# Optimization experiments

Measured on AMD Instinct MI355X. Metric: run time of the kernel, lower is better.

Reference implementation:

```python
import jax, jax.numpy as jnp
import numpy as np

D = 16  # feature (height) dim fixed by nn.Linear(16,16)

def setup_inputs() -> dict:
    key = jax.random.key(0)
    ks = jax.random.split(key, 7)
    B, C = 32, 1024
    inp = jax.random.normal(ks[0], (B, C, D), dtype=jnp.float32)
    s = 1.0 / np.sqrt(D)
    Wq = jax.random.uniform(ks[1], (D, D), jnp.float32, -s, s)
    bq = jax.random.uniform(ks[2], (D,), jnp.float32, -s, s)
    Wk = jax.random.uniform(ks[3], (D, D), jnp.float32, -s, s)
    bk = jax.random.uniform(ks[4], (D,), jnp.float32, -s, s)
    Wv = jax.random.uniform(ks[5], (D, D), jnp.float32, -s, s)
    bv = jax.random.uniform(ks[6], (D,), jnp.float32, -s, s)
    return {"input": inp, "Wq": Wq, "bq": bq, "Wk": Wk, "bk": bk, "Wv": Wv, "bv": bv}

def reference(input, Wq, bq, Wk, bk, Wv, bv):
    # torch Linear: y = x @ W.T + b
    Q = jnp.einsum('bcd,ed->bce', input, Wq) + bq  # [B,C,16]
    K = jnp.einsum('bcd,ed->bce', input, Wk) + bk
    V = jnp.einsum('bcd,ed->bce', input, Wv) + bv
    W = jnp.einsum('bqd,bkd->bqk', Q, K)           # [B,C,C], unscaled
    W = jax.nn.softmax(W, axis=2)
    att = jnp.einsum('bqk,bkd->bqd', W, V)         # [B,C,16]
    return att * input                              # elementwise gate
```

## Files before the change

### kernel.cpp

```cpp
#include <hip/hip_runtime.h>
#include <math.h>

#define DD 16
#define CC 1024
#define BB 32
#define QT 32

__global__ __launch_bounds__(256) void qkv_kernel(
    const float* __restrict__ x,
    const float* __restrict__ Wq, const float* __restrict__ bq,
    const float* __restrict__ Wk, const float* __restrict__ bk,
    const float* __restrict__ Wv, const float* __restrict__ bv,
    float* __restrict__ Q, float* __restrict__ K, float* __restrict__ V)
{
    __shared__ float xs[256 * DD];
    const int tid = threadIdx.x;
    const int m = blockIdx.y;
    const float* W    = (m == 0) ? Wq : (m == 1) ? Wk : Wv;
    const float* bias = (m == 0) ? bq : (m == 1) ? bk : bv;
    float*       O    = (m == 0) ? Q  : (m == 1) ? K  : V;

    const long base4 = (long)blockIdx.x * 256 * 4;
    const float4* x4 = (const float4*)x;
    float4* xs4 = (float4*)xs;
#pragma unroll
    for (int i = 0; i < 4; ++i)
        xs4[i * 256 + tid] = x4[base4 + i * 256 + tid];
    __syncthreads();

    float xr[16];
#pragma unroll
    for (int i = 0; i < 4; ++i) {
        float4 t = xs4[tid * 4 + i];
        xr[i*4+0] = t.x; xr[i*4+1] = t.y; xr[i*4+2] = t.z; xr[i*4+3] = t.w;
    }

    const long row = (long)blockIdx.x * 256 + tid;
    float4* O4 = (float4*)O;
#pragma unroll
    for (int g = 0; g < 4; ++g) {
        float o[4];
#pragma unroll
        for (int j = 0; j < 4; ++j) {
            const int e = g * 4 + j;
            float a = bias[e];
            const float* w = W + e * 16;
#pragma unroll
            for (int d = 0; d < 16; ++d) a = fmaf(xr[d], w[d], a);
            o[j] = a;
        }
        float4 ov; ov.x = o[0]; ov.y = o[1]; ov.z = o[2]; ov.w = o[3];
        O4[row * 4 + g] = ov;
    }
}

__global__ __launch_bounds__(256, 4) void attn_kernel(
    const float* __restrict__ Q, const float* __restrict__ K,
    const float* __restrict__ V, const float* __restrict__ x,
    float* __restrict__ out)
{
    __shared__ float smem[8192 + 256];
    float4* Ks4 = (float4*)smem;
    float4* Vs4 = (float4*)(smem + 4096);

    const int tid = threadIdx.x;
    const int q   = tid & 31;
    const int ks  = tid >> 5;
    const int b   = blockIdx.y;
    const int qbase = blockIdx.x * QT;
    const long qrow = (long)b * CC + qbase + q;

    const float4* Q4 = (const float4*)Q;
    float qr[16];
#pragma unroll
    for (int i = 0; i < 4; ++i) {
        float4 t = Q4[qrow * 4 + i];
        qr[i*4+0] = t.x; qr[i*4+1] = t.y; qr[i*4+2] = t.z; qr[i*4+3] = t.w;
    }

    float l = 0.f;
    float acc[16];
#pragma unroll
    for (int d = 0; d < 16; ++d) acc[d] = 0.f;

    const float4* K4 = (const float4*)K;
    const float4* V4 = (const float4*)V;

    for (int t = 0; t < 4; ++t) {
        const long tb4 = ((long)b * CC + t * 256) * 4;
        __syncthreads();
#pragma unroll
        for (int i = 0; i < 4; ++i) {
            Ks4[i * 256 + tid] = K4[tb4 + i * 256 + tid];
            Vs4[i * 256 + tid] = V4[tb4 + i * 256 + tid];
        }
        __syncthreads();

        const int k0 = ks * 32;
#pragma unroll 4
        for (int kk = 0; kk < 32; ++kk) {
            const int k = k0 + kk;
            float4 ka = Ks4[k * 4 + 0];
            float4 kb = Ks4[k * 4 + 1];
            float4 kc = Ks4[k * 4 + 2];
            float4 kd = Ks4[k * 4 + 3];
            float s = qr[0] * ka.x;
            s = fmaf(qr[1],  ka.y, s); s = fmaf(qr[2],  ka.z, s); s = fmaf(qr[3],  ka.w, s);
            s = fmaf(qr[4],  kb.x, s); s = fmaf(qr[5],  kb.y, s); s = fmaf(qr[6],  kb.z, s); s = fmaf(qr[7],  kb.w, s);
            s = fmaf(qr[8],  kc.x, s); s = fmaf(qr[9],  kc.y, s); s = fmaf(qr[10], kc.z, s); s = fmaf(qr[11], kc.w, s);
            s = fmaf(qr[12], kd.x, s); s = fmaf(qr[13], kd.y, s); s = fmaf(qr[14], kd.z, s); s = fmaf(qr[15], kd.w, s);

            const float p = __expf(s);
            l += p;

            float4 va = Vs4[k * 4 + 0];
            float4 vb = Vs4[k * 4 + 1];
            float4 vc = Vs4[k * 4 + 2];
            float4 vd = Vs4[k * 4 + 3];
            acc[0]  = fmaf(p, va.x, acc[0]);  acc[1]  = fmaf(p, va.y, acc[1]);
            acc[2]  = fmaf(p, va.z, acc[2]);  acc[3]  = fmaf(p, va.w, acc[3]);
            acc[4]  = fmaf(p, vb.x, acc[4]);  acc[5]  = fmaf(p, vb.y, acc[5]);
            acc[6]  = fmaf(p, vb.z, acc[6]);  acc[7]  = fmaf(p, vb.w, acc[7]);
            acc[8]  = fmaf(p, vc.x, acc[8]);  acc[9]  = fmaf(p, vc.y, acc[9]);
            acc[10] = fmaf(p, vc.z, acc[10]); acc[11] = fmaf(p, vc.w, acc[11]);
            acc[12] = fmaf(p, vd.x, acc[12]); acc[13] = fmaf(p, vd.y, acc[13]);
            acc[14] = fmaf(p, vd.z, acc[14]); acc[15] = fmaf(p, vd.w, acc[15]);
        }
    }

    __syncthreads();
    float* As = smem;
    float* Ls = smem + 8192;
    float4* As4 = (float4*)As;
#pragma unroll
    for (int i = 0; i < 4; ++i) {
        float4 t4;
        t4.x = acc[i*4+0]; t4.y = acc[i*4+1]; t4.z = acc[i*4+2]; t4.w = acc[i*4+3];
        As4[tid * 4 + i] = t4;
    }
    Ls[tid] = l;
    __syncthreads();

    if (tid < 128) {
        const int qq = tid & 31;
        const int dg = tid >> 5;
        float L = 0.f;
        float4 o; o.x = 0.f; o.y = 0.f; o.z = 0.f; o.w = 0.f;
#pragma unroll
        for (int s = 0; s < 8; ++s) {
            L += Ls[s * 32 + qq];
            float4 a = As4[(s * 32 + qq) * 4 + dg];
            o.x += a.x; o.y += a.y; o.z += a.z; o.w += a.w;
        }
        const float invL = 1.f / L;
        const long orow = (long)b * CC + qbase + qq;
        const float4 xg = ((const float4*)x)[orow * 4 + dg];
        float4 r;
        r.x = o.x * invL * xg.x;
        r.y = o.y * invL * xg.y;
        r.z = o.z * invL * xg.z;
        r.w = o.w * invL * xg.w;
        ((float4*)out)[orow * 4 + dg] = r;
    }
}

extern "C" void kernel_launch(void* const* d_in, const int* in_sizes, int n_in,
                              void* d_out, int out_size, void* d_ws, size_t ws_size,
                              hipStream_t stream) {
    const float* x  = (const float*)d_in[0];
    const float* Wq = (const float*)d_in[1];
    const float* bq = (const float*)d_in[2];
    const float* Wk = (const float*)d_in[3];
    const float* bk = (const float*)d_in[4];
    const float* Wv = (const float*)d_in[5];
    const float* bv = (const float*)d_in[6];
    float* out = (float*)d_out;

    const long n = (long)BB * CC * DD;
    float* Q = (float*)d_ws;
    float* K = Q + n;
    float* V = K + n;

    qkv_kernel<<<dim3((BB * CC) / 256, 3), dim3(256), 0, stream>>>(
        x, Wq, bq, Wk, bk, Wv, bv, Q, K, V);

    attn_kernel<<<dim3(CC / QT, BB), dim3(256), 0, stream>>>(Q, K, V, x, out);
}
```

Baseline: 116.3 us.

## Register-block four queries per thread and widen attention blocks to 512 threads

Each thread now keeps four query rows in registers, so every K and V row read from shared memory feeds four dot products and four accumulator updates instead of one. Blocks grow to 512 threads and 128 queries, with the 16 key-split warps walking keys in an interleaved order. This cuts LDS traffic per FLOP and reloads each K/V tile for fewer, larger blocks. In exchange it raises register pressure (64 accumulators plus 64 query values per thread), halves the occupancy hint, and turns the final reduction into four serialized shared-memory passes.

```diff
diff --git a/kernel.cpp b/kernel.cpp
--- a/kernel.cpp
+++ b/kernel.cpp
@@ -4,7 +4,8 @@
 #define DD 16
 #define CC 1024
 #define BB 32
-#define QT 32
+#define QT 128
+#define KT 256
 
 __global__ __launch_bounds__(256) void qkv_kernel(
     const float* __restrict__ x,
@@ -54,113 +55,135 @@
     }
 }
 
-__global__ __launch_bounds__(256, 4) void attn_kernel(
+__global__ __launch_bounds__(512, 2) void attn_kernel(
     const float* __restrict__ Q, const float* __restrict__ K,
     const float* __restrict__ V, const float* __restrict__ x,
     float* __restrict__ out)
 {
-    __shared__ float smem[8192 + 256];
+    __shared__ float smem[8192 + 512];
     float4* Ks4 = (float4*)smem;
     float4* Vs4 = (float4*)(smem + 4096);
 
     const int tid = threadIdx.x;
-    const int q   = tid & 31;
+    const int q32 = tid & 31;
     const int ks  = tid >> 5;
     const int b   = blockIdx.y;
     const int qbase = blockIdx.x * QT;
-    const long qrow = (long)b * CC + qbase + q;
 
     const float4* Q4 = (const float4*)Q;
-    float qr[16];
-#pragma unroll
-    for (int i = 0; i < 4; ++i) {
-        float4 t = Q4[qrow * 4 + i];
-        qr[i*4+0] = t.x; qr[i*4+1] = t.y; qr[i*4+2] = t.z; qr[i*4+3] = t.w;
-    }
-
-    float l = 0.f;
-    float acc[16];
-#pragma unroll
-    for (int d = 0; d < 16; ++d) acc[d] = 0.f;
+    float qr[4][16];
+#pragma unroll
+    for (int qb = 0; qb < 4; ++qb) {
+        const long row = (long)b * CC + qbase + qb * 32 + q32;
+#pragma unroll
+        for (int i = 0; i < 4; ++i) {
+            float4 t = Q4[row * 4 + i];
+            qr[qb][i*4+0] = t.x; qr[qb][i*4+1] = t.y;
+            qr[qb][i*4+2] = t.z; qr[qb][i*4+3] = t.w;
+        }
+    }
+
+    float lsum[4];
+    float acc[4][16];
+#pragma unroll
+    for (int qb = 0; qb < 4; ++qb) {
+        lsum[qb] = 0.f;
+#pragma unroll
+        for (int d = 0; d < 16; ++d) acc[qb][d] = 0.f;
+    }
 
     const float4* K4 = (const float4*)K;
     const float4* V4 = (const float4*)V;
 
     for (int t = 0; t < 4; ++t) {
-        const long tb4 = ((long)b * CC + t * 256) * 4;
-        __syncthreads();
-#pragma unroll
-        for (int i = 0; i < 4; ++i) {
-            Ks4[i * 256 + tid] = K4[tb4 + i * 256 + tid];
-            Vs4[i * 256 + tid] = V4[tb4 + i * 256 + tid];
-        }
-        __syncthreads();
-
-        const int k0 = ks * 32;
+        const long tb4 = ((long)b * CC + t * KT) * 4;
+        __syncthreads();
+        Ks4[tid]       = K4[tb4 + tid];
+        Ks4[tid + 512] = K4[tb4 + tid + 512];
+        Vs4[tid]       = V4[tb4 + tid];
+        Vs4[tid + 512] = V4[tb4 + tid + 512];
+        __syncthreads();
+
 #pragma unroll 4
-        for (int kk = 0; kk < 32; ++kk) {
-            const int k = k0 + kk;
-            float4 ka = Ks4[k * 4 + 0];
-            float4 kb = Ks4[k * 4 + 1];
-            float4 kc = Ks4[k * 4 + 2];
-            float4 kd = Ks4[k * 4 + 3];
-            float s = qr[0] * ka.x;
-            s = fmaf(qr[1],  ka.y, s); s = fmaf(qr[2],  ka.z, s); s = fmaf(qr[3],  ka.w, s);
-            s = fmaf(qr[4],  kb.x, s); s = fmaf(qr[5],  kb.y, s); s = fmaf(qr[6],  kb.z, s); s = fmaf(qr[7],  kb.w, s);
-            s = fmaf(qr[8],  kc.x, s); s = fmaf(qr[9],  kc.y, s); s = fmaf(qr[10], kc.z, s); s = fmaf(qr[11], kc.w, s);
-            s = fmaf(qr[12], kd.x, s); s = fmaf(qr[13], kd.y, s); s = fmaf(qr[14], kd.z, s); s = fmaf(qr[15], kd.w, s);
-
-            const float p = __expf(s);
-            l += p;
-
-            float4 va = Vs4[k * 4 + 0];
-            float4 vb = Vs4[k * 4 + 1];
-            float4 vc = Vs4[k * 4 + 2];
-            float4 vd = Vs4[k * 4 + 3];
-            acc[0]  = fmaf(p, va.x, acc[0]);  acc[1]  = fmaf(p, va.y, acc[1]);
-            acc[2]  = fmaf(p, va.z, acc[2]);  acc[3]  = fmaf(p, va.w, acc[3]);
-            acc[4]  = fmaf(p, vb.x, acc[4]);  acc[5]  = fmaf(p, vb.y, acc[5]);
-            acc[6]  = fmaf(p, vb.z, acc[6]);  acc[7]  = fmaf(p, vb.w, acc[7]);
-            acc[8]  = fmaf(p, vc.x, acc[8]);  acc[9]  = fmaf(p, vc.y, acc[9]);
-            acc[10] = fmaf(p, vc.z, acc[10]); acc[11] = fmaf(p, vc.w, acc[11]);
-            acc[12] = fmaf(p, vd.x, acc[12]); acc[13] = fmaf(p, vd.y, acc[13]);
-            acc[14] = fmaf(p, vd.z, acc[14]); acc[15] = fmaf(p, vd.w, acc[15]);
-        }
-    }
-
-    __syncthreads();
+        for (int kk = 0; kk < 16; ++kk) {
+            const int kl = (kk << 4) + ks;
+            const float4 ka = Ks4[kl * 4 + 0];
+            const float4 kb = Ks4[kl * 4 + 1];
+            const float4 kc = Ks4[kl * 4 + 2];
+            const float4 kd = Ks4[kl * 4 + 3];
+            float kr[16];
+            kr[0]=ka.x; kr[1]=ka.y; kr[2]=ka.z; kr[3]=ka.w;
+            kr[4]=kb.x; kr[5]=kb.y; kr[6]=kb.z; kr[7]=kb.w;
+            kr[8]=kc.x; kr[9]=kc.y; kr[10]=kc.z; kr[11]=kc.w;
+            kr[12]=kd.x; kr[13]=kd.y; kr[14]=kd.z; kr[15]=kd.w;
+
+            float p[4];
+#pragma unroll
+            for (int qb = 0; qb < 4; ++qb) {
+                float s = qr[qb][0] * kr[0];
+#pragma unroll
+                for (int d = 1; d < 16; ++d) s = fmaf(qr[qb][d], kr[d], s);
+                p[qb] = __expf(s);
+                lsum[qb] += p[qb];
+            }
+
+            const float4 va = Vs4[kl * 4 + 0];
+            const float4 vb = Vs4[kl * 4 + 1];
+            const float4 vc = Vs4[kl * 4 + 2];
+            const float4 vd = Vs4[kl * 4 + 3];
+            float vr[16];
+            vr[0]=va.x; vr[1]=va.y; vr[2]=va.z; vr[3]=va.w;
+            vr[4]=vb.x; vr[5]=vb.y; vr[6]=vb.z; vr[7]=vb.w;
+            vr[8]=vc.x; vr[9]=vc.y; vr[10]=vc.z; vr[11]=vc.w;
+            vr[12]=vd.x; vr[13]=vd.y; vr[14]=vd.z; vr[15]=vd.w;
+#pragma unroll
+            for (int qb = 0; qb < 4; ++qb)
+#pragma unroll
+                for (int d = 0; d < 16; ++d)
+                    acc[qb][d] = fmaf(p[qb], vr[d], acc[qb][d]);
+        }
+    }
+
     float* As = smem;
     float* Ls = smem + 8192;
     float4* As4 = (float4*)As;
-#pragma unroll
-    for (int i = 0; i < 4; ++i) {
-        float4 t4;
-        t4.x = acc[i*4+0]; t4.y = acc[i*4+1]; t4.z = acc[i*4+2]; t4.w = acc[i*4+3];
-        As4[tid * 4 + i] = t4;
-    }
-    Ls[tid] = l;
-    __syncthreads();
-
-    if (tid < 128) {
-        const int qq = tid & 31;
-        const int dg = tid >> 5;
-        float L = 0.f;
-        float4 o; o.x = 0.f; o.y = 0.f; o.z = 0.f; o.w = 0.f;
-#pragma unroll
-        for (int s = 0; s < 8; ++s) {
-            L += Ls[s * 32 + qq];
-            float4 a = As4[(s * 32 + qq) * 4 + dg];
-            o.x += a.x; o.y += a.y; o.z += a.z; o.w += a.w;
-        }
-        const float invL = 1.f / L;
-        const long orow = (long)b * CC + qbase + qq;
-        const float4 xg = ((const float4*)x)[orow * 4 + dg];
-        float4 r;
-        r.x = o.x * invL * xg.x;
-        r.y = o.y * invL * xg.y;
-        r.z = o.z * invL * xg.z;
-        r.w = o.w * invL * xg.w;
-        ((float4*)out)[orow * 4 + dg] = r;
+    const float4* x4 = (const float4*)x;
+    float4* out4 = (float4*)out;
+
+#pragma unroll
+    for (int qb = 0; qb < 4; ++qb) {
+        __syncthreads();
+#pragma unroll
+        for (int i = 0; i < 4; ++i) {
+            float4 t4;
+            t4.x = acc[qb][i*4+0]; t4.y = acc[qb][i*4+1];
+            t4.z = acc[qb][i*4+2]; t4.w = acc[qb][i*4+3];
+            As4[tid * 4 + i] = t4;
+        }
+        Ls[tid] = lsum[qb];
+        __syncthreads();
+
+        if (tid < 128) {
+            const int qq = tid >> 2;
+            const int dg = tid & 3;
+            float L = 0.f;
+            float4 o; o.x = 0.f; o.y = 0.f; o.z = 0.f; o.w = 0.f;
+#pragma unroll
+            for (int s = 0; s < 16; ++s) {
+                L += Ls[s * 32 + qq];
+                float4 a = As4[(s * 32 + qq) * 4 + dg];
+                o.x += a.x; o.y += a.y; o.z += a.z; o.w += a.w;
+            }
+            const float invL = 1.f / L;
+            const long orow = (long)b * CC + qbase + qb * 32 + qq;
+            const float4 xg = x4[orow * 4 + dg];
+            float4 r;
+            r.x = o.x * invL * xg.x;
+            r.y = o.y * invL * xg.y;
+            r.z = o.z * invL * xg.z;
+            r.w = o.w * invL * xg.w;
+            out4[orow * 4 + dg] = r;
+        }
     }
 }
 
@@ -184,5 +207,5 @@
     qkv_kernel<<<dim3((BB * CC) / 256, 3), dim3(256), 0, stream>>>(
         x, Wq, bq, Wk, bk, Wv, bv, Q, K, V);
 
-    attn_kernel<<<dim3(CC / QT, BB), dim3(256), 0, stream>>>(Q, K, V, x, out);
+    attn_kernel<<<dim3(CC / QT, BB), dim3(512), 0, stream>>>(Q, K, V, x, out);
 }
```

After: 108.5 us. -6.7%, faster.
